# Performance work log

Hardware: AMD Instinct MI355X
Metric: run time of the kernel (lower is better)

The kernel has to match this reference:

```python
import jax, jax.numpy as jnp
import numpy as np

N = 262144
H = 256
POS_L, DIR_L = 10, 4


def _encode(x, L):
    # classic NeRF sinusoidal encoding with identity: [N,3] -> [N, 3 + 6*L]
    f = 2.0 ** jnp.arange(L, dtype=x.dtype)          # [L]
    xf = x[:, :, None] * f                            # [N,3,L]
    n = x.shape[0]
    return jnp.concatenate([x, jnp.sin(xf).reshape(n, -1), jnp.cos(xf).reshape(n, -1)], axis=1)


def setup_inputs() -> dict:
    key = jax.random.key(0)
    ks = iter(jax.random.split(key, 32))
    inp = {
        "pos": jax.random.normal(next(ks), (N, 3), jnp.float32),
        "dir": jax.random.normal(next(ks), (N, 3), jnp.float32),
        "pixel_width": jax.random.uniform(next(ks), (N, 1), dtype=jnp.float32),
        "t_start": jax.random.uniform(next(ks), (N, 1), dtype=jnp.float32),
        "t_end": jax.random.uniform(next(ks), (N, 1), dtype=jnp.float32),
    }
    pe_dim = 3 + 6 * POS_L   # 63
    de_dim = 3 + 6 * DIR_L   # 27
    dims = {
        "w00": (pe_dim, H), "w01": (H, H), "w02": (H, H), "w03": (H, H),
        "w10": (H + pe_dim, H), "w11": (H, H), "w12": (H, H), "w13": (H, H),
        "cw0": (H + de_dim, H // 2), "cw1": (H // 2, 4),
    }
    for name, (i, o) in dims.items():
        inp[name] = jax.random.normal(next(ks), (i, o), jnp.float32) * (1.0 / np.sqrt(i))
        inp[name.replace("w", "b", 1)] = jnp.zeros((o,), jnp.float32)
    return inp


def _nerf(pos, dir, w00, b00, w01, b01, w02, b02, w03, b03,
          w10, b10, w11, b11, w12, b12, w13, b13, cw0, cb0, cw1, cb1):
    pe = _encode(pos, POS_L)   # [N,63]
    de = _encode(dir, DIR_L)   # [N,27]
    r = jax.nn.relu
    # segment 0 (4 linears, ReLU between all, plus inter-segment ReLU)
    z = r(pe @ w00 + b00)
    z = r(z @ w01 + b01)
    z = r(z @ w02 + b02)
    z = r(z @ w03 + b03)
    # segment 1: positional encoding re-concatenated (skip connection)
    z = jnp.concatenate([z, pe], axis=1)              # [N,319]
    z = r(z @ w10 + b10)
    z = r(z @ w11 + b11)
    z = r(z @ w12 + b12)
    z = z @ w13 + b13                                 # no activation after last segment
    # color head: direction encoding concatenated (delayed_direction=True)
    h = r(jnp.concatenate([z, de], axis=1) @ cw0 + cb0)   # [N,128]
    out = h @ cw1 + cb1                                    # [N,4] (rgb + density, delayed_density=True)
    d = out[:, -1]
    density = jnp.where(d > 8.0, d, jax.nn.softplus(d))    # Softplus(threshold=8)
    rgb = jax.nn.sigmoid(out[:, :3])
    return density, rgb


def reference(pos, dir, pixel_width, t_start, t_end,
              w00, b00, w01, b01, w02, b02, w03, b03,
              w10, b10, w11, b11, w12, b12, w13, b13,
              cw0, cb0, cw1, cb1):
    # pixel_width / t_start / t_end are consumed only by mip-style encoders; the
    # classic sinusoidal encoder used here ignores them (kept for signature parity).
    return _nerf(pos, dir, w00, b00, w01, b01, w02, b02, w03, b03,
                 w10, b10, w11, b11, w12, b12, w13, b13, cw0, cb0, cw1, cb1)
```

## Files before the change

kernel.cpp:

```cpp
#include <hip/hip_runtime.h>
#include <hip/hip_bf16.h>
#include <math.h>

typedef unsigned short u16;
typedef unsigned int   u32;
typedef __bf16 bf16x8 __attribute__((ext_vector_type(8)));
typedef float  f32x4  __attribute__((ext_vector_type(4)));

#define NRAYS 262144
#define NBLK  (NRAYS / 64)

enum : int { PO0=0, PO1=16384, PO2=81920, PO3=147456, PO4=212992,
             PO5=294912, PO6=360448, PO7=425984, PO8=491520, PO9=528384 };
#define TOTAL_PACK_ELEMS 530432

__device__ __forceinline__ u16 f2bf(float x) {
  return (u16)((__float_as_uint(x) + 0x8000u) >> 16);
}

struct PackArgs {
  const float* src[10];
  int K[10]; int N[10]; int l2mt[10]; int cstart[11];
};

__global__ __launch_bounds__(256) void pack_w(PackArgs a, u16* __restrict__ dst)
{
  int e = blockIdx.x * 256 + threadIdx.x;
  if (e >= TOTAL_PACK_ELEMS) return;
  int chunk = e >> 9;
  int li = 0;
  #pragma unroll
  for (int t = 1; t < 10; ++t) li += (chunk >= a.cstart[t]) ? 1 : 0;
  int lc = chunk - a.cstart[li];
  int ks = lc >> a.l2mt[li];
  int mt = lc - (ks << a.l2mt[li]);
  int lane = (e >> 3) & 63, j = e & 7;
  int k = ks * 32 + ((lane >> 4) << 3) + j;
  int n = mt * 16 + (lane & 15);
  float v = 0.f;
  if (k < a.K[li] && n < a.N[li]) v = a.src[li][(size_t)k * a.N[li] + n];
  u32 u = __float_as_uint(v);
  dst[e] = (u16)((u + 0x7FFFu + ((u >> 16) & 1u)) >> 16);
}

__device__ __forceinline__ void wr_enc(u16* zb, int r, int c, u16 v) {
  zb[r * 320 + ((((c >> 3) ^ (r & 7))) << 3) + (c & 7)] = v;
}

template<int MT_W>
__device__ __forceinline__ void binit(f32x4 acc[MT_W][4],
    const float* __restrict__ bias, int chbase, int lane)
{
  const int q = lane >> 4;
  #pragma unroll
  for (int mt = 0; mt < MT_W; ++mt) {
    float4 bv = *(const float4*)(bias + chbase + mt * 16 + q * 4);
    #pragma unroll
    for (int nt = 0; nt < 4; ++nt)
      acc[mt][nt] = (f32x4){bv.x, bv.y, bv.z, bv.w};
  }
}

template<int MT_W, int NSTEPS, int MT_TOTAL>
__device__ __forceinline__ void gseg(f32x4 acc[MT_W][4],
    const u16* __restrict__ zb, int cbase8,
    const u16* __restrict__ wl, int mt0, int ksbase, int lane)
{
  const int q = lane >> 4, llo = lane & 15;
  #pragma unroll
  for (int ks = 0; ks < NSTEPS; ++ks) {
    int c8s = ((cbase8 + ks * 4 + q) ^ (llo & 7));
    const u16* bp = zb + llo * 320 + c8s * 8;
    bf16x8 b[4];
    #pragma unroll
    for (int nt = 0; nt < 4; ++nt)
      b[nt] = *(const bf16x8*)(bp + nt * 16 * 320);
    int widx = ((ksbase + ks) * MT_TOTAL + mt0) * 512 + lane * 8;
    bf16x8 a[MT_W];
    #pragma unroll
    for (int mt = 0; mt < MT_W; ++mt)
      a[mt] = *(const bf16x8*)(wl + widx + mt * 512);
    #pragma unroll
    for (int mt = 0; mt < MT_W; ++mt)
      #pragma unroll
      for (int nt = 0; nt < 4; ++nt)
        acc[mt][nt] = __builtin_amdgcn_mfma_f32_16x16x32_bf16(a[mt], b[nt], acc[mt][nt], 0, 0, 0);
  }
}

template<int MT_W, bool RELU>
__device__ __forceinline__ void zstore(f32x4 acc[MT_W][4],
    int chbase, u16* zb, int lane)
{
  const int llo = lane & 15, q = lane >> 4;
  #pragma unroll
  for (int mt = 0; mt < MT_W; ++mt) {
    int ch = chbase + mt * 16 + q * 4;
    int off0 = (((ch >> 3) ^ (llo & 7)) << 3) + (ch & 7);
    #pragma unroll
    for (int nt = 0; nt < 4; ++nt) {
      f32x4 v = acc[mt][nt];
      float x0 = v.x, x1 = v.y, x2 = v.z, x3 = v.w;
      if (RELU) { x0 = fmaxf(x0, 0.f); x1 = fmaxf(x1, 0.f);
                  x2 = fmaxf(x2, 0.f); x3 = fmaxf(x3, 0.f); }
      u32 a0 = __float_as_uint(x0) + 0x8000u;
      u32 a1 = __float_as_uint(x1) + 0x8000u;
      u32 a2 = __float_as_uint(x2) + 0x8000u;
      u32 a3 = __float_as_uint(x3) + 0x8000u;
      uint2 pk;
      pk.x = (a1 & 0xFFFF0000u) | (a0 >> 16);
      pk.y = (a3 & 0xFFFF0000u) | (a2 >> 16);
      *(uint2*)(zb + (nt * 16 + llo) * 320 + off0) = pk;
    }
  }
}

__global__ __launch_bounds__(256, 3) void nerf_fused(
    const float* __restrict__ pos,  const float* __restrict__ dirv,
    const float* __restrict__ b00,  const float* __restrict__ b01,
    const float* __restrict__ b02,  const float* __restrict__ b03,
    const float* __restrict__ b10,  const float* __restrict__ b11,
    const float* __restrict__ b12,  const float* __restrict__ b13,
    const float* __restrict__ cb0,  const float* __restrict__ cb1,
    const u16* __restrict__ W, float* __restrict__ out)
{
  __shared__ __align__(16) u16 zb[64 * 320];
  float* xyzf = (float*)zb;

  const int tid = threadIdx.x;
  const int rb  = blockIdx.x * 64;
  const int lane = tid & 63, wid = tid >> 6;

  if (tid < 192) {
    int r = tid / 3, c = tid - r * 3;
    xyzf[r * 160 + c] = pos[(size_t)(rb + r) * 3 + c];
  }
  __syncthreads();

  #pragma unroll
  for (int i = tid; i < 64 * 32; i += 256) {
    int r = i >> 5, t = i & 31;
    if (t < 30) {
      int j = t / 10, l = t - j * 10;
      float x = xyzf[r * 160 + j] * (float)(1 << l);
      wr_enc(zb, r, 256 + 3 + t,  f2bf(__sinf(x)));
      wr_enc(zb, r, 256 + 33 + t, f2bf(__cosf(x)));
    }
  }
  {
    int r = tid >> 2, c = tid & 3;
    u16 v = 0; int col = 63;
    if (c < 3) { col = c; v = f2bf(xyzf[r * 160 + c]); }
    wr_enc(zb, r, 256 + col, v);
  }
  __syncthreads();

  f32x4 acc[4][4];

  binit<4>(acc, b00, wid * 64, lane);
  gseg<4, 2, 16>(acc, zb, 32, W + PO0, wid * 4, 0, lane);
  __syncthreads();
  zstore<4, true>(acc, wid * 64, zb, lane);
  __syncthreads();
  binit<4>(acc, b01, wid * 64, lane);
  gseg<4, 8, 16>(acc, zb, 0, W + PO1, wid * 4, 0, lane);
  __syncthreads();
  zstore<4, true>(acc, wid * 64, zb, lane);
  __syncthreads();
  binit<4>(acc, b02, wid * 64, lane);
  gseg<4, 8, 16>(acc, zb, 0, W + PO2, wid * 4, 0, lane);
  __syncthreads();
  zstore<4, true>(acc, wid * 64, zb, lane);
  __syncthreads();
  binit<4>(acc, b03, wid * 64, lane);
  gseg<4, 8, 16>(acc, zb, 0, W + PO3, wid * 4, 0, lane);
  __syncthreads();
  zstore<4, true>(acc, wid * 64, zb, lane);
  __syncthreads();
  binit<4>(acc, b10, wid * 64, lane);
  gseg<4, 8, 16>(acc, zb, 0,  W + PO4, wid * 4, 0, lane);
  gseg<4, 2, 16>(acc, zb, 32, W + PO4, wid * 4, 8, lane);
  __syncthreads();
  zstore<4, true>(acc, wid * 64, zb, lane);
  #pragma unroll
  for (int i = tid; i < 64 * 16; i += 256) {
    int r = i >> 4, t = i & 15;
    if (t < 12) {
      int j = t >> 2, l = t & 3;
      float x = dirv[(size_t)(rb + r) * 3 + j] * (float)(1 << l);
      wr_enc(zb, r, 288 + 3 + t,  f2bf(__sinf(x)));
      wr_enc(zb, r, 288 + 15 + t, f2bf(__cosf(x)));
    } else {
      wr_enc(zb, r, 288 + 15 + t, 0);
    }
  }
  {
    int r = tid >> 2, c = tid & 3;
    u16 v = 0; int col = 31;
    if (c < 3) { col = c; v = f2bf(dirv[(size_t)(rb + r) * 3 + c]); }
    wr_enc(zb, r, 288 + col, v);
  }
  __syncthreads();
  binit<4>(acc, b11, wid * 64, lane);
  gseg<4, 8, 16>(acc, zb, 0, W + PO5, wid * 4, 0, lane);
  __syncthreads();
  zstore<4, true>(acc, wid * 64, zb, lane);
  __syncthreads();
  binit<4>(acc, b12, wid * 64, lane);
  gseg<4, 8, 16>(acc, zb, 0, W + PO6, wid * 4, 0, lane);
  __syncthreads();
  zstore<4, true>(acc, wid * 64, zb, lane);
  __syncthreads();
  binit<4>(acc, b13, wid * 64, lane);
  gseg<4, 8, 16>(acc, zb, 0, W + PO7, wid * 4, 0, lane);
  __syncthreads();
  zstore<4, false>(acc, wid * 64, zb, lane);
  __syncthreads();
  {
    f32x4 acc2[2][4];
    binit<2>(acc2, cb0, wid * 32, lane);
    gseg<2, 8, 8>(acc2, zb, 0,  W + PO8, wid * 2, 0, lane);
    gseg<2, 1, 8>(acc2, zb, 36, W + PO8, wid * 2, 8, lane);
    __syncthreads();
    zstore<2, true>(acc2, wid * 32, zb, lane);
    __syncthreads();
  }
  {
    const u16* W9 = W + PO9;
    const int q = lane >> 4, llo = lane & 15;
    const int r = wid * 16 + llo;
    f32x4 c9 = (f32x4){0.f, 0.f, 0.f, 0.f};
    #pragma unroll
    for (int ks = 0; ks < 4; ++ks) {
      int c8s = ((ks * 4 + q) ^ (llo & 7));
      bf16x8 b = *(const bf16x8*)(zb + r * 320 + c8s * 8);
      bf16x8 a = *(const bf16x8*)(W9 + ks * 512 + lane * 8);
      c9 = __builtin_amdgcn_mfma_f32_16x16x32_bf16(a, b, c9, 0, 0, 0);
    }
    if (q == 0) {
      int ray = rb + r;
      float o0 = c9.x + cb1[0];
      float o1 = c9.y + cb1[1];
      float o2 = c9.z + cb1[2];
      float dv = c9.w + cb1[3];
      out[ray] = (dv > 8.f) ? dv : log1pf(__expf(dv));
      float* rgb = out + NRAYS + (size_t)ray * 3;
      rgb[0] = 1.f / (1.f + __expf(-o0));
      rgb[1] = 1.f / (1.f + __expf(-o1));
      rgb[2] = 1.f / (1.f + __expf(-o2));
    }
  }
}

extern "C" void kernel_launch(void* const* d_in, const int* in_sizes, int n_in,
                              void* d_out, int out_size, void* d_ws, size_t ws_size,
                              hipStream_t stream)
{
  (void)in_sizes; (void)n_in; (void)out_size; (void)ws_size;
  const float* pos  = (const float*)d_in[0];
  const float* dirv = (const float*)d_in[1];
  PackArgs pa;
  const int widx[10] = {5, 7, 9, 11, 13, 15, 17, 19, 21, 23};
  const int K[10]    = {63, 256, 256, 256, 319, 256, 256, 256, 283, 128};
  const int Nn[10]   = {256, 256, 256, 256, 256, 256, 256, 256, 128, 4};
  const int L2MT[10] = {4, 4, 4, 4, 4, 4, 4, 4, 3, 0};
  const int CS[11]   = {0, 32, 160, 288, 416, 576, 704, 832, 960, 1032, 1036};
  for (int i = 0; i < 10; ++i) {
    pa.src[i] = (const float*)d_in[widx[i]];
    pa.K[i] = K[i]; pa.N[i] = Nn[i]; pa.l2mt[i] = L2MT[i];
  }
  for (int i = 0; i < 11; ++i) pa.cstart[i] = CS[i];

  u16* wp = (u16*)d_ws;
  hipLaunchKernelGGL(pack_w, dim3(TOTAL_PACK_ELEMS / 256), dim3(256), 0, stream, pa, wp);

  hipLaunchKernelGGL(nerf_fused, dim3(NBLK), dim3(256), 0, stream,
      pos, dirv,
      (const float*)d_in[6],  (const float*)d_in[8],
      (const float*)d_in[10], (const float*)d_in[12],
      (const float*)d_in[14], (const float*)d_in[16],
      (const float*)d_in[18], (const float*)d_in[20],
      (const float*)d_in[22], (const float*)d_in[24],
      wp, (float*)d_out);
}
```

Before: 354.7 us.

## Switch fused NeRF MLP GEMMs from 16x16x32 to 32x32x16 bf16 MFMA

```diff
diff --git a/kernel.cpp b/kernel.cpp
--- a/kernel.cpp
+++ b/kernel.cpp
@@ -6,6 +6,7 @@
 typedef unsigned int   u32;
 typedef __bf16 bf16x8 __attribute__((ext_vector_type(8)));
 typedef float  f32x4  __attribute__((ext_vector_type(4)));
+typedef float  f32x16 __attribute__((ext_vector_type(16)));
 
 #define NRAYS 262144
 #define NBLK  (NRAYS / 64)
@@ -35,8 +36,14 @@
   int ks = lc >> a.l2mt[li];
   int mt = lc - (ks << a.l2mt[li]);
   int lane = (e >> 3) & 63, j = e & 7;
-  int k = ks * 32 + ((lane >> 4) << 3) + j;
-  int n = mt * 16 + (lane & 15);
+  int k, n;
+  if (li == 9) {
+    k = ks * 32 + ((lane >> 4) << 3) + j;
+    n = lane & 15;
+  } else {
+    k = ks * 16 + ((lane >> 5) << 3) + j;
+    n = mt * 32 + (lane & 31);
+  }
   float v = 0.f;
   if (k < a.K[li] && n < a.N[li]) v = a.src[li][(size_t)k * a.N[li] + n];
   u32 u = __float_as_uint(v);
@@ -48,69 +55,77 @@
 }
 
 template<int MT_W>
-__device__ __forceinline__ void binit(f32x4 acc[MT_W][4],
+__device__ __forceinline__ void binit32(f32x16 acc[MT_W][2],
     const float* __restrict__ bias, int chbase, int lane)
 {
-  const int q = lane >> 4;
-  #pragma unroll
-  for (int mt = 0; mt < MT_W; ++mt) {
-    float4 bv = *(const float4*)(bias + chbase + mt * 16 + q * 4);
-    #pragma unroll
-    for (int nt = 0; nt < 4; ++nt)
-      acc[mt][nt] = (f32x4){bv.x, bv.y, bv.z, bv.w};
-  }
+  const int q5 = lane >> 5;
+  #pragma unroll
+  for (int mt = 0; mt < MT_W; ++mt)
+    #pragma unroll
+    for (int g = 0; g < 4; ++g) {
+      float4 bv = *(const float4*)(bias + chbase + mt * 32 + 8 * g + 4 * q5);
+      #pragma unroll
+      for (int nt = 0; nt < 2; ++nt) {
+        acc[mt][nt][4*g+0] = bv.x; acc[mt][nt][4*g+1] = bv.y;
+        acc[mt][nt][4*g+2] = bv.z; acc[mt][nt][4*g+3] = bv.w;
+      }
+    }
 }
 
 template<int MT_W, int NSTEPS, int MT_TOTAL>
-__device__ __forceinline__ void gseg(f32x4 acc[MT_W][4],
+__device__ __forceinline__ void gseg32(f32x16 acc[MT_W][2],
     const u16* __restrict__ zb, int cbase8,
     const u16* __restrict__ wl, int mt0, int ksbase, int lane)
 {
-  const int q = lane >> 4, llo = lane & 15;
+  const int q5 = lane >> 5, l5 = lane & 31;
+  const u16* brow = zb + l5 * 320;
   #pragma unroll
   for (int ks = 0; ks < NSTEPS; ++ks) {
-    int c8s = ((cbase8 + ks * 4 + q) ^ (llo & 7));
-    const u16* bp = zb + llo * 320 + c8s * 8;
-    bf16x8 b[4];
-    #pragma unroll
-    for (int nt = 0; nt < 4; ++nt)
-      b[nt] = *(const bf16x8*)(bp + nt * 16 * 320);
-    int widx = ((ksbase + ks) * MT_TOTAL + mt0) * 512 + lane * 8;
+    int c8 = (cbase8 + ks * 2 + q5) ^ (l5 & 7);
+    const u16* bp = brow + c8 * 8;
+    bf16x8 b0 = *(const bf16x8*)(bp);
+    bf16x8 b1 = *(const bf16x8*)(bp + 32 * 320);
+    const u16* wp = wl + ((ksbase + ks) * MT_TOTAL + mt0) * 512 + lane * 8;
     bf16x8 a[MT_W];
     #pragma unroll
     for (int mt = 0; mt < MT_W; ++mt)
-      a[mt] = *(const bf16x8*)(wl + widx + mt * 512);
-    #pragma unroll
-    for (int mt = 0; mt < MT_W; ++mt)
+      a[mt] = *(const bf16x8*)(wp + mt * 512);
+    #pragma unroll
+    for (int mt = 0; mt < MT_W; ++mt) {
+      acc[mt][0] = __builtin_amdgcn_mfma_f32_32x32x16_bf16(a[mt], b0, acc[mt][0], 0, 0, 0);
+      acc[mt][1] = __builtin_amdgcn_mfma_f32_32x32x16_bf16(a[mt], b1, acc[mt][1], 0, 0, 0);
+    }
+  }
+}
+
+template<int MT_W, bool RELU>
+__device__ __forceinline__ void zstore32(f32x16 acc[MT_W][2],
+    int chbase, u16* zb, int lane)
+{
+  const int l5 = lane & 31, q5 = lane >> 5;
+  #pragma unroll
+  for (int mt = 0; mt < MT_W; ++mt) {
+    #pragma unroll
+    for (int nt = 0; nt < 2; ++nt) {
+      int row = nt * 32 + l5;
+      u16* rp = zb + row * 320;
       #pragma unroll
-      for (int nt = 0; nt < 4; ++nt)
-        acc[mt][nt] = __builtin_amdgcn_mfma_f32_16x16x32_bf16(a[mt], b[nt], acc[mt][nt], 0, 0, 0);
-  }
-}
-
-template<int MT_W, bool RELU>
-__device__ __forceinline__ void zstore(f32x4 acc[MT_W][4],
-    int chbase, u16* zb, int lane)
-{
-  const int llo = lane & 15, q = lane >> 4;
-  #pragma unroll
-  for (int mt = 0; mt < MT_W; ++mt) {
-    int ch = chbase + mt * 16 + q * 4;
-    int off0 = (((ch >> 3) ^ (llo & 7)) << 3) + (ch & 7);
-    #pragma unroll
-    for (int nt = 0; nt < 4; ++nt) {
-      f32x4 v = acc[mt][nt];
-      float x0 = v.x, x1 = v.y, x2 = v.z, x3 = v.w;
-      if (RELU) { x0 = fmaxf(x0, 0.f); x1 = fmaxf(x1, 0.f);
-                  x2 = fmaxf(x2, 0.f); x3 = fmaxf(x3, 0.f); }
-      u32 a0 = __float_as_uint(x0) + 0x8000u;
-      u32 a1 = __float_as_uint(x1) + 0x8000u;
-      u32 a2 = __float_as_uint(x2) + 0x8000u;
-      u32 a3 = __float_as_uint(x3) + 0x8000u;
-      uint2 pk;
-      pk.x = (a1 & 0xFFFF0000u) | (a0 >> 16);
-      pk.y = (a3 & 0xFFFF0000u) | (a2 >> 16);
-      *(uint2*)(zb + (nt * 16 + llo) * 320 + off0) = pk;
+      for (int g = 0; g < 4; ++g) {
+        int ch = chbase + mt * 32 + 8 * g + 4 * q5;
+        int off = (((ch >> 3) ^ (l5 & 7)) << 3) + (ch & 7);
+        float x0 = acc[mt][nt][4*g+0], x1 = acc[mt][nt][4*g+1];
+        float x2 = acc[mt][nt][4*g+2], x3 = acc[mt][nt][4*g+3];
+        if (RELU) { x0 = fmaxf(x0, 0.f); x1 = fmaxf(x1, 0.f);
+                    x2 = fmaxf(x2, 0.f); x3 = fmaxf(x3, 0.f); }
+        u32 a0 = __float_as_uint(x0) + 0x8000u;
+        u32 a1 = __float_as_uint(x1) + 0x8000u;
+        u32 a2 = __float_as_uint(x2) + 0x8000u;
+        u32 a3 = __float_as_uint(x3) + 0x8000u;
+        uint2 pk;
+        pk.x = (a1 & 0xFFFF0000u) | (a0 >> 16);
+        pk.y = (a3 & 0xFFFF0000u) | (a2 >> 16);
+        *(uint2*)(rp + off) = pk;
+      }
     }
   }
 }
@@ -155,33 +170,33 @@
   }
   __syncthreads();
 
-  f32x4 acc[4][4];
-
-  binit<4>(acc, b00, wid * 64, lane);
-  gseg<4, 2, 16>(acc, zb, 32, W + PO0, wid * 4, 0, lane);
-  __syncthreads();
-  zstore<4, true>(acc, wid * 64, zb, lane);
-  __syncthreads();
-  binit<4>(acc, b01, wid * 64, lane);
-  gseg<4, 8, 16>(acc, zb, 0, W + PO1, wid * 4, 0, lane);
-  __syncthreads();
-  zstore<4, true>(acc, wid * 64, zb, lane);
-  __syncthreads();
-  binit<4>(acc, b02, wid * 64, lane);
-  gseg<4, 8, 16>(acc, zb, 0, W + PO2, wid * 4, 0, lane);
-  __syncthreads();
-  zstore<4, true>(acc, wid * 64, zb, lane);
-  __syncthreads();
-  binit<4>(acc, b03, wid * 64, lane);
-  gseg<4, 8, 16>(acc, zb, 0, W + PO3, wid * 4, 0, lane);
-  __syncthreads();
-  zstore<4, true>(acc, wid * 64, zb, lane);
-  __syncthreads();
-  binit<4>(acc, b10, wid * 64, lane);
-  gseg<4, 8, 16>(acc, zb, 0,  W + PO4, wid * 4, 0, lane);
-  gseg<4, 2, 16>(acc, zb, 32, W + PO4, wid * 4, 8, lane);
-  __syncthreads();
-  zstore<4, true>(acc, wid * 64, zb, lane);
+  f32x16 acc[2][2];
+
+  binit32<2>(acc, b00, wid * 64, lane);
+  gseg32<2, 4, 8>(acc, zb, 32, W + PO0, wid * 2, 0, lane);
+  __syncthreads();
+  zstore32<2, true>(acc, wid * 64, zb, lane);
+  __syncthreads();
+  binit32<2>(acc, b01, wid * 64, lane);
+  gseg32<2, 16, 8>(acc, zb, 0, W + PO1, wid * 2, 0, lane);
+  __syncthreads();
+  zstore32<2, true>(acc, wid * 64, zb, lane);
+  __syncthreads();
+  binit32<2>(acc, b02, wid * 64, lane);
+  gseg32<2, 16, 8>(acc, zb, 0, W + PO2, wid * 2, 0, lane);
+  __syncthreads();
+  zstore32<2, true>(acc, wid * 64, zb, lane);
+  __syncthreads();
+  binit32<2>(acc, b03, wid * 64, lane);
+  gseg32<2, 16, 8>(acc, zb, 0, W + PO3, wid * 2, 0, lane);
+  __syncthreads();
+  zstore32<2, true>(acc, wid * 64, zb, lane);
+  __syncthreads();
+  binit32<2>(acc, b10, wid * 64, lane);
+  gseg32<2, 16, 8>(acc, zb, 0,  W + PO4, wid * 2, 0,  lane);
+  gseg32<2, 4,  8>(acc, zb, 32, W + PO4, wid * 2, 16, lane);
+  __syncthreads();
+  zstore32<2, true>(acc, wid * 64, zb, lane);
   #pragma unroll
   for (int i = tid; i < 64 * 16; i += 256) {
     int r = i >> 4, t = i & 15;
@@ -201,28 +216,28 @@
     wr_enc(zb, r, 288 + col, v);
   }
   __syncthreads();
-  binit<4>(acc, b11, wid * 64, lane);
-  gseg<4, 8, 16>(acc, zb, 0, W + PO5, wid * 4, 0, lane);
-  __syncthreads();
-  zstore<4, true>(acc, wid * 64, zb, lane);
-  __syncthreads();
-  binit<4>(acc, b12, wid * 64, lane);
-  gseg<4, 8, 16>(acc, zb, 0, W + PO6, wid * 4, 0, lane);
-  __syncthreads();
-  zstore<4, true>(acc, wid * 64, zb, lane);
-  __syncthreads();
-  binit<4>(acc, b13, wid * 64, lane);
-  gseg<4, 8, 16>(acc, zb, 0, W + PO7, wid * 4, 0, lane);
-  __syncthreads();
-  zstore<4, false>(acc, wid * 64, zb, lane);
+  binit32<2>(acc, b11, wid * 64, lane);
+  gseg32<2, 16, 8>(acc, zb, 0, W + PO5, wid * 2, 0, lane);
+  __syncthreads();
+  zstore32<2, true>(acc, wid * 64, zb, lane);
+  __syncthreads();
+  binit32<2>(acc, b12, wid * 64, lane);
+  gseg32<2, 16, 8>(acc, zb, 0, W + PO6, wid * 2, 0, lane);
+  __syncthreads();
+  zstore32<2, true>(acc, wid * 64, zb, lane);
+  __syncthreads();
+  binit32<2>(acc, b13, wid * 64, lane);
+  gseg32<2, 16, 8>(acc, zb, 0, W + PO7, wid * 2, 0, lane);
+  __syncthreads();
+  zstore32<2, false>(acc, wid * 64, zb, lane);
   __syncthreads();
   {
-    f32x4 acc2[2][4];
-    binit<2>(acc2, cb0, wid * 32, lane);
-    gseg<2, 8, 8>(acc2, zb, 0,  W + PO8, wid * 2, 0, lane);
-    gseg<2, 1, 8>(acc2, zb, 36, W + PO8, wid * 2, 8, lane);
+    f32x16 acc8[1][2];
+    binit32<1>(acc8, cb0, wid * 32, lane);
+    gseg32<1, 16, 4>(acc8, zb, 0,  W + PO8, wid, 0,  lane);
+    gseg32<1, 2,  4>(acc8, zb, 36, W + PO8, wid, 16, lane);
     __syncthreads();
-    zstore<2, true>(acc2, wid * 32, zb, lane);
+    zstore32<1, true>(acc8, wid * 32, zb, lane);
     __syncthreads();
   }
   {
@@ -263,7 +278,7 @@
   const int widx[10] = {5, 7, 9, 11, 13, 15, 17, 19, 21, 23};
   const int K[10]    = {63, 256, 256, 256, 319, 256, 256, 256, 283, 128};
   const int Nn[10]   = {256, 256, 256, 256, 256, 256, 256, 256, 128, 4};
-  const int L2MT[10] = {4, 4, 4, 4, 4, 4, 4, 4, 3, 0};
+  const int L2MT[10] = {3, 3, 3, 3, 3, 3, 3, 3, 2, 0};
   const int CS[11]   = {0, 32, 160, 288, 416, 576, 704, 832, 960, 1032, 1036};
   for (int i = 0; i < 10; ++i) {
     pa.src[i] = (const float*)d_in[widx[i]];
```

Result: slower. 394.7 us (+11.3%).

## Ping-pong activation buffers and use 8 waves per block to halve barriers

Applied to the files above, without the earlier changes.

```diff
diff --git a/kernel.cpp b/kernel.cpp
--- a/kernel.cpp
+++ b/kernel.cpp
@@ -43,10 +43,6 @@
   dst[e] = (u16)((u + 0x7FFFu + ((u >> 16) & 1u)) >> 16);
 }
 
-__device__ __forceinline__ void wr_enc(u16* zb, int r, int c, u16 v) {
-  zb[r * 320 + ((((c >> 3) ^ (r & 7))) << 3) + (c & 7)] = v;
-}
-
 template<int MT_W>
 __device__ __forceinline__ void binit(f32x4 acc[MT_W][4],
     const float* __restrict__ bias, int chbase, int lane)
@@ -61,7 +57,7 @@
   }
 }
 
-template<int MT_W, int NSTEPS, int MT_TOTAL>
+template<int MT_W, int NSTEPS, int MT_TOTAL, int STRIDE>
 __device__ __forceinline__ void gseg(f32x4 acc[MT_W][4],
     const u16* __restrict__ zb, int cbase8,
     const u16* __restrict__ wl, int mt0, int ksbase, int lane)
@@ -70,16 +66,16 @@
   #pragma unroll
   for (int ks = 0; ks < NSTEPS; ++ks) {
     int c8s = ((cbase8 + ks * 4 + q) ^ (llo & 7));
-    const u16* bp = zb + llo * 320 + c8s * 8;
+    const u16* bp = zb + llo * STRIDE + c8s * 8;
     bf16x8 b[4];
     #pragma unroll
     for (int nt = 0; nt < 4; ++nt)
-      b[nt] = *(const bf16x8*)(bp + nt * 16 * 320);
-    int widx = ((ksbase + ks) * MT_TOTAL + mt0) * 512 + lane * 8;
+      b[nt] = *(const bf16x8*)(bp + nt * 16 * STRIDE);
+    const u16* wp = wl + ((ksbase + ks) * MT_TOTAL + mt0) * 512 + lane * 8;
     bf16x8 a[MT_W];
     #pragma unroll
     for (int mt = 0; mt < MT_W; ++mt)
-      a[mt] = *(const bf16x8*)(wl + widx + mt * 512);
+      a[mt] = *(const bf16x8*)(wp + mt * 512);
     #pragma unroll
     for (int mt = 0; mt < MT_W; ++mt)
       #pragma unroll
@@ -90,7 +86,7 @@
 
 template<int MT_W, bool RELU>
 __device__ __forceinline__ void zstore(f32x4 acc[MT_W][4],
-    int chbase, u16* zb, int lane)
+    int chbase, u16* dst, int lane)
 {
   const int llo = lane & 15, q = lane >> 4;
   #pragma unroll
@@ -110,12 +106,17 @@
       uint2 pk;
       pk.x = (a1 & 0xFFFF0000u) | (a0 >> 16);
       pk.y = (a3 & 0xFFFF0000u) | (a2 >> 16);
-      *(uint2*)(zb + (nt * 16 + llo) * 320 + off0) = pk;
-    }
-  }
-}
-
-__global__ __launch_bounds__(256, 3) void nerf_fused(
+      *(uint2*)(dst + (nt * 16 + llo) * 256 + off0) = pk;
+    }
+  }
+}
+
+__device__ __forceinline__ void wr_pe(u16* peb, int r, int c, u16 v) {
+  peb[r * 64 + (((c >> 3) ^ (r & 7)) << 3) + (c & 7)];
+  peb[r * 64 + (((c >> 3) ^ (r & 7)) << 3) + (c & 7)] = v;
+}
+
+__global__ __launch_bounds__(512, 4) void nerf_fused(
     const float* __restrict__ pos,  const float* __restrict__ dirv,
     const float* __restrict__ b00,  const float* __restrict__ b01,
     const float* __restrict__ b02,  const float* __restrict__ b03,
@@ -124,8 +125,10 @@
     const float* __restrict__ cb0,  const float* __restrict__ cb1,
     const u16* __restrict__ W, float* __restrict__ out)
 {
-  __shared__ __align__(16) u16 zb[64 * 320];
-  float* xyzf = (float*)zb;
+  __shared__ __align__(16) u16 zA[64 * 256];
+  __shared__ __align__(16) u16 zB[64 * 256];
+  __shared__ __align__(16) u16 peb[64 * 64];
+  float* xyzf = (float*)zB;
 
   const int tid = threadIdx.x;
   const int rb  = blockIdx.x * 64;
@@ -133,99 +136,89 @@
 
   if (tid < 192) {
     int r = tid / 3, c = tid - r * 3;
-    xyzf[r * 160 + c] = pos[(size_t)(rb + r) * 3 + c];
-  }
-  __syncthreads();
-
-  #pragma unroll
-  for (int i = tid; i < 64 * 32; i += 256) {
-    int r = i >> 5, t = i & 31;
-    if (t < 30) {
-      int j = t / 10, l = t - j * 10;
-      float x = xyzf[r * 160 + j] * (float)(1 << l);
-      wr_enc(zb, r, 256 + 3 + t,  f2bf(__sinf(x)));
-      wr_enc(zb, r, 256 + 33 + t, f2bf(__cosf(x)));
-    }
-  }
-  {
+    xyzf[r * 8 + c] = pos[(size_t)(rb + r) * 3 + c];
+  }
+  __syncthreads();
+
+  #pragma unroll
+  for (int i = tid; i < 64 * 30; i += 512) {
+    int r = i / 30, t = i - r * 30;
+    int j = t / 10, l = t - j * 10;
+    float x = xyzf[r * 8 + j] * (float)(1 << l);
+    wr_pe(peb, r, 3 + t,  f2bf(__sinf(x)));
+    wr_pe(peb, r, 33 + t, f2bf(__cosf(x)));
+  }
+  if (tid < 256) {
     int r = tid >> 2, c = tid & 3;
     u16 v = 0; int col = 63;
-    if (c < 3) { col = c; v = f2bf(xyzf[r * 160 + c]); }
-    wr_enc(zb, r, 256 + col, v);
-  }
-  __syncthreads();
-
-  f32x4 acc[4][4];
-
-  binit<4>(acc, b00, wid * 64, lane);
-  gseg<4, 2, 16>(acc, zb, 32, W + PO0, wid * 4, 0, lane);
-  __syncthreads();
-  zstore<4, true>(acc, wid * 64, zb, lane);
-  __syncthreads();
-  binit<4>(acc, b01, wid * 64, lane);
-  gseg<4, 8, 16>(acc, zb, 0, W + PO1, wid * 4, 0, lane);
-  __syncthreads();
-  zstore<4, true>(acc, wid * 64, zb, lane);
-  __syncthreads();
-  binit<4>(acc, b02, wid * 64, lane);
-  gseg<4, 8, 16>(acc, zb, 0, W + PO2, wid * 4, 0, lane);
-  __syncthreads();
-  zstore<4, true>(acc, wid * 64, zb, lane);
-  __syncthreads();
-  binit<4>(acc, b03, wid * 64, lane);
-  gseg<4, 8, 16>(acc, zb, 0, W + PO3, wid * 4, 0, lane);
-  __syncthreads();
-  zstore<4, true>(acc, wid * 64, zb, lane);
-  __syncthreads();
-  binit<4>(acc, b10, wid * 64, lane);
-  gseg<4, 8, 16>(acc, zb, 0,  W + PO4, wid * 4, 0, lane);
-  gseg<4, 2, 16>(acc, zb, 32, W + PO4, wid * 4, 8, lane);
-  __syncthreads();
-  zstore<4, true>(acc, wid * 64, zb, lane);
-  #pragma unroll
-  for (int i = tid; i < 64 * 16; i += 256) {
+    if (c < 3) { col = c; v = f2bf(xyzf[r * 8 + c]); }
+    wr_pe(peb, r, col, v);
+  }
+  __syncthreads();
+
+  f32x4 acc[2][4];
+  const int mt0 = wid * 2, chb = wid * 32;
+
+  binit<2>(acc, b00, chb, lane);
+  gseg<2, 2, 16, 64>(acc, peb, 0, W + PO0, mt0, 0, lane);
+  zstore<2, true>(acc, chb, zA, lane);
+  __syncthreads();
+  binit<2>(acc, b01, chb, lane);
+  gseg<2, 8, 16, 256>(acc, zA, 0, W + PO1, mt0, 0, lane);
+  zstore<2, true>(acc, chb, zB, lane);
+  __syncthreads();
+  binit<2>(acc, b02, chb, lane);
+  gseg<2, 8, 16, 256>(acc, zB, 0, W + PO2, mt0, 0, lane);
+  zstore<2, true>(acc, chb, zA, lane);
+  __syncthreads();
+  binit<2>(acc, b03, chb, lane);
+  gseg<2, 8, 16, 256>(acc, zA, 0, W + PO3, mt0, 0, lane);
+  zstore<2, true>(acc, chb, zB, lane);
+  __syncthreads();
+  binit<2>(acc, b10, chb, lane);
+  gseg<2, 8, 16, 256>(acc, zB, 0, W + PO4, mt0, 0, lane);
+  gseg<2, 2, 16, 64>(acc, peb, 0, W + PO4, mt0, 8, lane);
+  zstore<2, true>(acc, chb, zA, lane);
+  __syncthreads();
+  #pragma unroll
+  for (int i = tid; i < 64 * 16; i += 512) {
     int r = i >> 4, t = i & 15;
     if (t < 12) {
       int j = t >> 2, l = t & 3;
       float x = dirv[(size_t)(rb + r) * 3 + j] * (float)(1 << l);
-      wr_enc(zb, r, 288 + 3 + t,  f2bf(__sinf(x)));
-      wr_enc(zb, r, 288 + 15 + t, f2bf(__cosf(x)));
+      wr_pe(peb, r, 32 + 3 + t,  f2bf(__sinf(x)));
+      wr_pe(peb, r, 32 + 15 + t, f2bf(__cosf(x)));
     } else {
-      wr_enc(zb, r, 288 + 15 + t, 0);
-    }
-  }
-  {
+      wr_pe(peb, r, 32 + 15 + t, 0);
+    }
+  }
+  if (tid < 256) {
     int r = tid >> 2, c = tid & 3;
     u16 v = 0; int col = 31;
     if (c < 3) { col = c; v = f2bf(dirv[(size_t)(rb + r) * 3 + c]); }
-    wr_enc(zb, r, 288 + col, v);
-  }
-  __syncthreads();
-  binit<4>(acc, b11, wid * 64, lane);
-  gseg<4, 8, 16>(acc, zb, 0, W + PO5, wid * 4, 0, lane);
-  __syncthreads();
-  zstore<4, true>(acc, wid * 64, zb, lane);
-  __syncthreads();
-  binit<4>(acc, b12, wid * 64, lane);
-  gseg<4, 8, 16>(acc, zb, 0, W + PO6, wid * 4, 0, lane);
-  __syncthreads();
-  zstore<4, true>(acc, wid * 64, zb, lane);
-  __syncthreads();
-  binit<4>(acc, b13, wid * 64, lane);
-  gseg<4, 8, 16>(acc, zb, 0, W + PO7, wid * 4, 0, lane);
-  __syncthreads();
-  zstore<4, false>(acc, wid * 64, zb, lane);
+    wr_pe(peb, r, 32 + col, v);
+  }
+  binit<2>(acc, b11, chb, lane);
+  gseg<2, 8, 16, 256>(acc, zA, 0, W + PO5, mt0, 0, lane);
+  zstore<2, true>(acc, chb, zB, lane);
+  __syncthreads();
+  binit<2>(acc, b12, chb, lane);
+  gseg<2, 8, 16, 256>(acc, zB, 0, W + PO6, mt0, 0, lane);
+  zstore<2, true>(acc, chb, zA, lane);
+  __syncthreads();
+  binit<2>(acc, b13, chb, lane);
+  gseg<2, 8, 16, 256>(acc, zA, 0, W + PO7, mt0, 0, lane);
+  zstore<2, false>(acc, chb, zB, lane);
   __syncthreads();
   {
-    f32x4 acc2[2][4];
-    binit<2>(acc2, cb0, wid * 32, lane);
-    gseg<2, 8, 8>(acc2, zb, 0,  W + PO8, wid * 2, 0, lane);
-    gseg<2, 1, 8>(acc2, zb, 36, W + PO8, wid * 2, 8, lane);
+    f32x4 acc8[1][4];
+    binit<1>(acc8, cb0, wid * 16, lane);
+    gseg<1, 8, 8, 256>(acc8, zB, 0, W + PO8, wid, 0, lane);
+    gseg<1, 1, 8, 64>(acc8, peb, 4, W + PO8, wid, 8, lane);
+    zstore<1, true>(acc8, wid * 16, zA, lane);
     __syncthreads();
-    zstore<2, true>(acc2, wid * 32, zb, lane);
-    __syncthreads();
-  }
-  {
+  }
+  if (wid < 4) {
     const u16* W9 = W + PO9;
     const int q = lane >> 4, llo = lane & 15;
     const int r = wid * 16 + llo;
@@ -233,7 +226,7 @@
     #pragma unroll
     for (int ks = 0; ks < 4; ++ks) {
       int c8s = ((ks * 4 + q) ^ (llo & 7));
-      bf16x8 b = *(const bf16x8*)(zb + r * 320 + c8s * 8);
+      bf16x8 b = *(const bf16x8*)(zA + r * 256 + c8s * 8);
       bf16x8 a = *(const bf16x8*)(W9 + ks * 512 + lane * 8);
       c9 = __builtin_amdgcn_mfma_f32_16x16x32_bf16(a, b, c9, 0, 0, 0);
     }
@@ -274,7 +267,7 @@
   u16* wp = (u16*)d_ws;
   hipLaunchKernelGGL(pack_w, dim3(TOTAL_PACK_ELEMS / 256), dim3(256), 0, stream, pa, wp);
 
-  hipLaunchKernelGGL(nerf_fused, dim3(NBLK), dim3(256), 0, stream,
+  hipLaunchKernelGGL(nerf_fused, dim3(NBLK), dim3(512), 0, stream,
       pos, dirv,
       (const float*)d_in[6],  (const float*)d_in[8],
       (const float*)d_in[10], (const float*)d_in[12],
```

Result: no change. 361.3 us (+1.9%).
